# Performance work log

Hardware: AMD Instinct MI355X
Metric: run time of the kernel (lower is better)

Reference implementation:

```python
import jax, jax.numpy as jnp
import numpy as np

NUM_NODES = 10000


def setup_inputs() -> dict:
    key = jax.random.key(0)
    k1, k2, k3, k4 = jax.random.split(key, 4)
    x = jax.random.normal(k1, (NUM_NODES, 128), dtype=jnp.float32)
    edge_index = jax.random.randint(k2, (2, 640000), 0, NUM_NODES, dtype=jnp.int64)
    W = jax.random.normal(k3, (128, 128), dtype=jnp.float32) * (1.0 / np.sqrt(128))
    b = jax.random.normal(k4, (128,), dtype=jnp.float32) * 0.01
    return {"x": x, "edge_index": edge_index, "W": W, "b": b}


def reference(x, edge_index, W, b):
    src, dst = edge_index[0], edge_index[1]
    num_nodes = x.shape[0]
    # scatter-add: aggregated[dst] += x[src]
    aggregated = jax.ops.segment_sum(x[src], dst, num_segments=num_nodes)
    # in-degree normalization (clamped at 1)
    degree = jax.ops.segment_sum(jnp.ones_like(dst, dtype=x.dtype), dst,
                                 num_segments=num_nodes)
    degree = jnp.maximum(degree, 1.0)
    aggregated = aggregated / degree[:, None]
    # linear (y = h @ W.T + b) + ReLU
    out = jax.nn.relu(jnp.einsum('nd,od->no', aggregated + x, W) + b)
    return out
```

## Files before the change

### kernel.cpp

```cpp
#include <hip/hip_runtime.h>
#include <hip/hip_bf16.h>

#define NB    256
#define EPB   2500
#define NPAD  10240
#define NPT   40
#define NGEMM 625
#define LCAP  1024

typedef __bf16 bf16_8 __attribute__((ext_vector_type(8)));
typedef float f32_4 __attribute__((ext_vector_type(4)));
typedef float f32_8 __attribute__((ext_vector_type(8)));

__global__ void __launch_bounds__(256) k_fused(
    const float* __restrict__ x, const float* __restrict__ W,
    const int* __restrict__ ei, int E,
    __hip_bfloat16* __restrict__ zb, unsigned short* __restrict__ bins,
    unsigned int* __restrict__ combo) {
  __shared__ int h[NPAD / 2];
  __shared__ unsigned short sorted[EPB];
  __shared__ int wsum[4];

  if (blockIdx.x < NGEMM) {
    int rowbase = blockIdx.x * 16;
    int wid = threadIdx.x >> 6;
    int lane = threadIdx.x & 63;
    int m16 = lane & 15;
    int quad = lane >> 4;

    union { bf16_8 v; __hip_bfloat16 h8[8]; } ac[4];
    const float* arow = x + (size_t)(rowbase + m16) * 128 + quad * 8;
#pragma unroll
    for (int kk = 0; kk < 4; ++kk) {
      f32_8 af = *(const f32_8*)(arow + kk * 32);
#pragma unroll
      for (int j = 0; j < 8; ++j) ac[kk].h8[j] = __float2bfloat16(af[j]);
    }
#pragma unroll
    for (int ct = 0; ct < 2; ++ct) {
      int colbase = wid * 32 + ct * 16;
      const float* brow = W + (size_t)(colbase + m16) * 128 + quad * 8;
      f32_4 c = {0.f, 0.f, 0.f, 0.f};
#pragma unroll
      for (int kk = 0; kk < 4; ++kk) {
        f32_8 bf = *(const f32_8*)(brow + kk * 32);
        union { bf16_8 v; __hip_bfloat16 h8[8]; } bc;
#pragma unroll
        for (int j = 0; j < 8; ++j) bc.h8[j] = __float2bfloat16(bf[j]);
        c = __builtin_amdgcn_mfma_f32_16x16x32_bf16(ac[kk].v, bc.v, c, 0, 0, 0);
      }
#pragma unroll
      for (int r = 0; r < 4; ++r) {
        int row = rowbase + quad * 4 + r;
        zb[(size_t)row * 128 + colbase + m16] = __float2bfloat16(c[r]);
      }
    }
    return;
  }

  const int b = blockIdx.x - NGEMM;
  const int t = threadIdx.x;
  const int4* src4 = (const int4*)(ei) + b * (EPB / 4);
  const int4* dst4 = (const int4*)(ei + E) + b * (EPB / 4);

  for (int i = t; i < NPAD / 2; i += 256) h[i] = 0;
  __syncthreads();

  for (int i = t; i < EPB / 4; i += 256) {
    int4 d = dst4[i];
    atomicAdd(&h[d.x >> 1], 1 << ((d.x & 1) * 16));
    atomicAdd(&h[d.y >> 1], 1 << ((d.y & 1) * 16));
    atomicAdd(&h[d.z >> 1], 1 << ((d.z & 1) * 16));
    atomicAdd(&h[d.w >> 1], 1 << ((d.w & 1) * 16));
  }
  __syncthreads();

  int raw[NPT];
  const int lo = t * NPT;
  int sum = 0;
#pragma unroll
  for (int j = 0; j < NPT; j += 2) {
    int pair = h[(lo + j) >> 1];
    raw[j] = pair & 0xFFFF;
    raw[j + 1] = (pair >> 16) & 0xFFFF;
    sum += raw[j] + raw[j + 1];
  }
  int incl = sum;
#pragma unroll
  for (int off = 1; off < 64; off <<= 1) {
    int v = __shfl_up(incl, off);
    if ((t & 63) >= off) incl += v;
  }
  if ((t & 63) == 63) wsum[t >> 6] = incl;
  __syncthreads();
  int wb = 0;
  for (int w = 0; w < (t >> 6); ++w) wb += wsum[w];
  int run = wb + incl - sum;

  unsigned int cpack[NPT];
#pragma unroll
  for (int j = 0; j < NPT; j += 2) {
    int r0 = run; run += raw[j];
    int r1 = run; run += raw[j + 1];
    h[(lo + j) >> 1] = (r1 << 16) | r0;
    cpack[j]     = ((unsigned)raw[j] << 16) | (unsigned)r0;
    cpack[j + 1] = ((unsigned)raw[j + 1] << 16) | (unsigned)r1;
  }
  __syncthreads();

  unsigned int* crow = combo + (size_t)b * NPAD + lo;
#pragma unroll
  for (int j = 0; j < NPT; j += 4)
    *(uint4*)(crow + j) = make_uint4(cpack[j], cpack[j+1], cpack[j+2], cpack[j+3]);

  for (int i = t; i < EPB / 4; i += 256) {
    int4 s4 = src4[i];
    int4 d4 = dst4[i];
    int ss[4] = {s4.x, s4.y, s4.z, s4.w};
    int dd[4] = {d4.x, d4.y, d4.z, d4.w};
#pragma unroll
    for (int u = 0; u < 4; ++u) {
      int n = dd[u];
      int sh = (n & 1) * 16;
      int pos = (atomicAdd(&h[n >> 1], 1 << sh) >> sh) & 0xFFFF;
      sorted[pos] = (unsigned short)ss[u];
    }
  }
  __syncthreads();

  unsigned int* outb = (unsigned int*)(bins + (size_t)b * EPB);
  const unsigned int* s32 = (const unsigned int*)sorted;
  for (int i = t; i < EPB / 2; i += 256) outb[i] = s32[i];
}

__global__ void __launch_bounds__(256) k_agg(
    const unsigned int* __restrict__ combo, const unsigned short* __restrict__ bins,
    const __hip_bfloat16* __restrict__ zb, const float* __restrict__ bias,
    float* __restrict__ out, int N) {
  __shared__ unsigned int trans[4][256];
  __shared__ unsigned short list[4][LCAP];
  __shared__ int cursor[4];

  const int t = threadIdx.x;
  const int wid = t >> 6;
  const int lane = t & 63;
  const int n0 = blockIdx.x * 4;

  if (t < 4) cursor[t] = 0;
  uint4 cm = *(const uint4*)(combo + (size_t)t * NPAD + n0);
  trans[0][t] = cm.x; trans[1][t] = cm.y; trans[2][t] = cm.z; trans[3][t] = cm.w;
  __syncthreads();

  const int n = n0 + wid;
  uint4 cc = *(const uint4*)&trans[wid][4 * lane];
  int cs[4] = {(int)(cc.x >> 16), (int)(cc.y >> 16), (int)(cc.z >> 16), (int)(cc.w >> 16)};
  int os[4] = {(int)(cc.x & 0xFFFF), (int)(cc.y & 0xFFFF), (int)(cc.z & 0xFFFF), (int)(cc.w & 0xFFFF)};
  int tot = cs[0] + cs[1] + cs[2] + cs[3];

  int p = atomicAdd(&cursor[wid], tot);

  {
    int q = p;
#pragma unroll
    for (int k = 0; k < 4; ++k) {
      int c = cs[k];
      const unsigned short* bk = bins + (size_t)(4 * lane + k) * EPB + os[k];
      unsigned short s0 = 0, s1 = 0, s2 = 0;
      if (c > 0) s0 = bk[0];
      if (c > 1) s1 = bk[1];
      if (c > 2) s2 = bk[2];
      if (c > 0 && q < LCAP) list[wid][q] = s0;
      if (c > 1 && q + 1 < LCAP) list[wid][q + 1] = s1;
      if (c > 2 && q + 2 < LCAP) list[wid][q + 2] = s2;
      for (int j = 3; j < c; ++j)
        if (q + j < LCAP) list[wid][q + j] = bk[j];
      q += c;
    }
  }
  __syncthreads();

  const int m = cursor[wid];
  const int g = lane >> 4;
  const int sub = lane & 15;
  int mm = m < LCAP ? m : LCAP;

  float acc[8] = {0.f, 0.f, 0.f, 0.f, 0.f, 0.f, 0.f, 0.f};
  for (int e = 0; e < mm; e += 32) {
#pragma unroll
    for (int u = 0; u < 8; ++u) {
      int idx = e + u * 4 + g;
      if (idx < mm) {
        int s = list[wid][idx];
        bf16_8 v = *(const bf16_8*)(zb + (size_t)s * 128 + sub * 8);
#pragma unroll
        for (int k = 0; k < 8; ++k) acc[k] += (float)v[k];
      }
    }
  }
#pragma unroll
  for (int k = 0; k < 8; ++k) {
    acc[k] += __shfl_xor(acc[k], 16);
    acc[k] += __shfl_xor(acc[k], 32);
  }

  if (g == 0 && n < N) {
    float inv = 1.f / (float)(m > 0 ? m : 1);
    bf16_8 zn = *(const bf16_8*)(zb + (size_t)n * 128 + sub * 8);
    f32_8 bv = *(const f32_8*)(bias + sub * 8);
    float r[8];
#pragma unroll
    for (int k = 0; k < 8; ++k) {
      float v = acc[k] * inv + (float)zn[k] + bv[k];
      r[k] = v > 0.f ? v : 0.f;
    }
    float* o = out + (size_t)n * 128 + sub * 8;
    *(float4*)(o)     = make_float4(r[0], r[1], r[2], r[3]);
    *(float4*)(o + 4) = make_float4(r[4], r[5], r[6], r[7]);
  }
}

extern "C" void kernel_launch(void* const* d_in, const int* in_sizes, int n_in,
                              void* d_out, int out_size, void* d_ws, size_t ws_size,
                              hipStream_t stream) {
  const float* x = (const float*)d_in[0];
  const int* ei = (const int*)d_in[1];
  const float* W = (const float*)d_in[2];
  const float* b = (const float*)d_in[3];
  float* out = (float*)d_out;

  const int N = in_sizes[0] / 128;
  const int E = in_sizes[1] / 2;

  char* ws = (char*)d_ws;
  size_t off = 0;
  auto carve = [&](size_t bytes) {
    void* p = ws + off;
    off = (off + bytes + 255) & ~(size_t)255;
    return p;
  };
  __hip_bfloat16* zb = (__hip_bfloat16*)carve((size_t)N * 128 * 2);
  unsigned short* bins = (unsigned short*)carve((size_t)NB * EPB * 2);
  unsigned int* combo = (unsigned int*)carve((size_t)NB * NPAD * 4);

  k_fused<<<NGEMM + NB, 256, 0, stream>>>(x, W, ei, E, zb, bins, combo);
  k_agg<<<N / 4, 256, 0, stream>>>(combo, bins, zb, b, out, N);
}
```

Baseline: 108.6 us.

## Transpose per-bin offset table and make neighbor gather branch-free with in-flight loads

The per-bin count/offset table is now written node-major, so each aggregation wave reads its node's 256 entries with one contiguous load instead of staging a transpose through shared memory. The neighbor list stores precomputed byte offsets and is padded to a multiple of 32 with entries pointing at an extra zeroed row of the bf16 buffer. That lets the gather issue eight unconditional vector loads before accumulating, which removes the per-element branch and keeps more memory requests in flight. In exchange, the binning kernel now does strided 4-byte stores to the table, the list cap drops to 256 entries per node, and a block-wide barrier is removed in favor of wave-local ordering.

```diff
diff --git a/kernel.cpp b/kernel.cpp
--- a/kernel.cpp
+++ b/kernel.cpp
@@ -6,7 +6,8 @@
 #define NPAD  10240
 #define NPT   40
 #define NGEMM 625
-#define LCAP  1024
+#define LCAP  256
+#define ZOFF  (10000u * 256u)
 
 typedef __bf16 bf16_8 __attribute__((ext_vector_type(8)));
 typedef float f32_4 __attribute__((ext_vector_type(4)));
@@ -21,6 +22,12 @@
   __shared__ unsigned short sorted[EPB];
   __shared__ int wsum[4];
 
+  if (blockIdx.x == NGEMM + NB) {
+    if (threadIdx.x < 32)
+      ((uint2*)(zb + (size_t)10000 * 128))[threadIdx.x] = make_uint2(0u, 0u);
+    return;
+  }
+
   if (blockIdx.x < NGEMM) {
     int rowbase = blockIdx.x * 16;
     int wid = threadIdx.x >> 6;
@@ -97,21 +104,15 @@
   for (int w = 0; w < (t >> 6); ++w) wb += wsum[w];
   int run = wb + incl - sum;
 
-  unsigned int cpack[NPT];
 #pragma unroll
   for (int j = 0; j < NPT; j += 2) {
     int r0 = run; run += raw[j];
     int r1 = run; run += raw[j + 1];
     h[(lo + j) >> 1] = (r1 << 16) | r0;
-    cpack[j]     = ((unsigned)raw[j] << 16) | (unsigned)r0;
-    cpack[j + 1] = ((unsigned)raw[j + 1] << 16) | (unsigned)r1;
-  }
-  __syncthreads();
-
-  unsigned int* crow = combo + (size_t)b * NPAD + lo;
-#pragma unroll
-  for (int j = 0; j < NPT; j += 4)
-    *(uint4*)(crow + j) = make_uint4(cpack[j], cpack[j+1], cpack[j+2], cpack[j+3]);
+    combo[(size_t)(lo + j) * NB + b]     = ((unsigned)raw[j] << 16) | (unsigned)r0;
+    combo[(size_t)(lo + j + 1) * NB + b] = ((unsigned)raw[j + 1] << 16) | (unsigned)r1;
+  }
+  __syncthreads();
 
   for (int i = t; i < EPB / 4; i += 256) {
     int4 s4 = src4[i];
@@ -137,22 +138,18 @@
     const unsigned int* __restrict__ combo, const unsigned short* __restrict__ bins,
     const __hip_bfloat16* __restrict__ zb, const float* __restrict__ bias,
     float* __restrict__ out, int N) {
-  __shared__ unsigned int trans[4][256];
-  __shared__ unsigned short list[4][LCAP];
+  __shared__ unsigned int list[4][LCAP];
   __shared__ int cursor[4];
 
   const int t = threadIdx.x;
   const int wid = t >> 6;
   const int lane = t & 63;
-  const int n0 = blockIdx.x * 4;
+  const int n = blockIdx.x * 4 + wid;
 
   if (t < 4) cursor[t] = 0;
-  uint4 cm = *(const uint4*)(combo + (size_t)t * NPAD + n0);
-  trans[0][t] = cm.x; trans[1][t] = cm.y; trans[2][t] = cm.z; trans[3][t] = cm.w;
-  __syncthreads();
-
-  const int n = n0 + wid;
-  uint4 cc = *(const uint4*)&trans[wid][4 * lane];
+  __syncthreads();
+
+  uint4 cc = *(const uint4*)(combo + (size_t)n * NB + 4 * lane);
   int cs[4] = {(int)(cc.x >> 16), (int)(cc.y >> 16), (int)(cc.z >> 16), (int)(cc.w >> 16)};
   int os[4] = {(int)(cc.x & 0xFFFF), (int)(cc.y & 0xFFFF), (int)(cc.z & 0xFFFF), (int)(cc.w & 0xFFFF)};
   int tot = cs[0] + cs[1] + cs[2] + cs[3];
@@ -169,33 +166,36 @@
       if (c > 0) s0 = bk[0];
       if (c > 1) s1 = bk[1];
       if (c > 2) s2 = bk[2];
-      if (c > 0 && q < LCAP) list[wid][q] = s0;
-      if (c > 1 && q + 1 < LCAP) list[wid][q + 1] = s1;
-      if (c > 2 && q + 2 < LCAP) list[wid][q + 2] = s2;
+      if (c > 0 && q < LCAP) list[wid][q] = (unsigned)s0 << 8;
+      if (c > 1 && q + 1 < LCAP) list[wid][q + 1] = (unsigned)s1 << 8;
+      if (c > 2 && q + 2 < LCAP) list[wid][q + 2] = (unsigned)s2 << 8;
       for (int j = 3; j < c; ++j)
-        if (q + j < LCAP) list[wid][q + j] = bk[j];
+        if (q + j < LCAP) list[wid][q + j] = (unsigned)bk[j] << 8;
       q += c;
     }
   }
-  __syncthreads();
 
   const int m = cursor[wid];
+  int mm = m < LCAP ? m : LCAP;
+  int mpad = (mm + 31) & ~31;
+  for (int j = mm + lane; j < mpad; j += 64) list[wid][j] = ZOFF;
+
   const int g = lane >> 4;
   const int sub = lane & 15;
-  int mm = m < LCAP ? m : LCAP;
+  const char* zbase = (const char*)zb + sub * 16;
 
   float acc[8] = {0.f, 0.f, 0.f, 0.f, 0.f, 0.f, 0.f, 0.f};
-  for (int e = 0; e < mm; e += 32) {
-#pragma unroll
-    for (int u = 0; u < 8; ++u) {
-      int idx = e + u * 4 + g;
-      if (idx < mm) {
-        int s = list[wid][idx];
-        bf16_8 v = *(const bf16_8*)(zb + (size_t)s * 128 + sub * 8);
-#pragma unroll
-        for (int k = 0; k < 8; ++k) acc[k] += (float)v[k];
-      }
-    }
+  for (int e = 0; e < mpad; e += 32) {
+    unsigned int offs[8];
+#pragma unroll
+    for (int u = 0; u < 8; ++u) offs[u] = list[wid][e + u * 4 + g];
+    bf16_8 v[8];
+#pragma unroll
+    for (int u = 0; u < 8; ++u) v[u] = *(const bf16_8*)(zbase + offs[u]);
+#pragma unroll
+    for (int u = 0; u < 8; ++u)
+#pragma unroll
+      for (int k = 0; k < 8; ++k) acc[k] += (float)v[u][k];
   }
 #pragma unroll
   for (int k = 0; k < 8; ++k) {
@@ -210,8 +210,8 @@
     float r[8];
 #pragma unroll
     for (int k = 0; k < 8; ++k) {
-      float v = acc[k] * inv + (float)zn[k] + bv[k];
-      r[k] = v > 0.f ? v : 0.f;
+      float v2 = acc[k] * inv + (float)zn[k] + bv[k];
+      r[k] = v2 > 0.f ? v2 : 0.f;
     }
     float* o = out + (size_t)n * 128 + sub * 8;
     *(float4*)(o)     = make_float4(r[0], r[1], r[2], r[3]);
@@ -238,10 +238,10 @@
     off = (off + bytes + 255) & ~(size_t)255;
     return p;
   };
-  __hip_bfloat16* zb = (__hip_bfloat16*)carve((size_t)N * 128 * 2);
+  __hip_bfloat16* zb = (__hip_bfloat16*)carve((size_t)(N + 1) * 128 * 2);
   unsigned short* bins = (unsigned short*)carve((size_t)NB * EPB * 2);
-  unsigned int* combo = (unsigned int*)carve((size_t)NB * NPAD * 4);
-
-  k_fused<<<NGEMM + NB, 256, 0, stream>>>(x, W, ei, E, zb, bins, combo);
+  unsigned int* combo = (unsigned int*)carve((size_t)NPAD * NB * 4);
+
+  k_fused<<<NGEMM + NB + 1, 256, 0, stream>>>(x, W, ei, E, zb, bins, combo);
   k_agg<<<N / 4, 256, 0, stream>>>(combo, bins, zb, b, out, N);
 }
```

Result: slower. 112.2 us (+3.3%).
